# Optimization experiments

Measured on AMD Instinct MI355X. Metric: run time of the kernel, lower is better.

Reference implementation:

```python
import jax, jax.numpy as jnp
import numpy as np

NEG_SLOPE = 0.2  # init arg negative_slope


def setup_inputs() -> dict:
    key = jax.random.key(0)
    k1, k2, k3, k4 = jax.random.split(key, 4)
    N, E, D_IN, D_OUT = 8192, 262144, 128, 128
    h = jax.random.normal(k1, (N, D_IN), dtype=jnp.float32)
    edge_index = jax.random.randint(k2, (2, E), 0, N, dtype=jnp.int64)
    # nn.Linear(in, out, bias=False) weight: [out, in]
    W = jax.random.normal(k3, (D_OUT, D_IN), dtype=jnp.float32) * (1.0 / np.sqrt(D_IN))
    # att parameter: [2*out, 1], xavier-uniform-ish scale
    lim = np.sqrt(6.0 / (2 * D_OUT + 1)) * 1.414
    att = jax.random.uniform(k4, (2 * D_OUT, 1), dtype=jnp.float32, minval=-lim, maxval=lim)
    return {"h": h, "edge_index": edge_index, "W": W, "att": att}


def reference(h, edge_index, W, att):
    # h: [N, d_in], edge_index: [2, E], W: [d_out, d_in], att: [2*d_out, 1]
    h_trans = h @ W.T                                  # [N, d_out]
    row, col = edge_index[0], edge_index[1]
    e = jnp.concatenate([h_trans[row], h_trans[col]], axis=1)  # [E, 2*d_out]
    edge_e = jnp.squeeze(e @ att, axis=-1)             # [E]
    edge_e = jnp.where(edge_e >= 0, edge_e, NEG_SLOPE * edge_e)  # leaky_relu
    N = h.shape[0]
    attention = jnp.zeros((N, N), dtype=h_trans.dtype).at[row, col].set(edge_e)
    attention = (attention + attention.T) * 0.5        # symmetrize
    fill_value = edge_e.max()                          # .item() -> constant (no grad)
    diag = jnp.arange(N)
    attention = attention.at[diag, diag].set(fill_value)
    attention = jax.nn.softmax(attention, axis=1)      # row softmax over dense NxN
    h_prime = attention @ h_trans                      # [N, d_out]
    h_prime = jax.nn.elu(h_prime)                      # concat=True -> ELU
    # F.dropout in eval mode is identity
    return h_prime, attention
```

## Files before the change

kernel.cpp:

```cpp
#include <hip/hip_runtime.h>
#include <stdint.h>

#define NN 8192
#define EE 262144
#define DD 128
#define NEGS 0.2f
#define HBITS 20
#define HSIZE (1<<HBITS)
#define HMASK (HSIZE-1)
#define BCAP 256

typedef float f32x4 __attribute__((ext_vector_type(4)));

__device__ __forceinline__ unsigned f2ord(float f){
  unsigned u = __float_as_uint(f);
  return (u & 0x80000000u) ? ~u : (u | 0x80000000u);
}
__device__ __forceinline__ float ord2f(unsigned u){
  return __uint_as_float((u & 0x80000000u) ? (u & 0x7fffffffu) : ~u);
}
__device__ __forceinline__ unsigned hmix(int key){
  unsigned h = (unsigned)key * 2654435761u;
  h ^= h >> 15;
  return h;
}

__global__ void k_setup(int* hkeys, int* hvals, int* cnt, float* T,
                        unsigned* fillmax, const float* __restrict__ W,
                        float* __restrict__ wt){
  int gid = blockIdx.x*256 + threadIdx.x;
  int4 m1 = {-1,-1,-1,-1};
  if(gid < HSIZE/4)            ((int4*)hkeys)[gid] = m1;
  else if(gid < HSIZE/2)       ((int4*)hvals)[gid - HSIZE/4] = m1;
  if(gid < NN/4)               ((int4*)cnt)[gid] = int4{0,0,0,0};
  if(gid < DD/4)               ((float4*)T)[gid] = float4{0.f,0.f,0.f,0.f};
  if(gid == 0)                 *fillmax = 0x007FFFFFu;
  if(gid < DD*DD){
    int c = gid >> 7, k = gid & 127;
    wt[k*DD + c] = W[gid];
  }
}

__global__ __launch_bounds__(256) void k_gemm(const float* __restrict__ h,
                                              const float* __restrict__ wt,
                                              float* __restrict__ ht){
  __shared__ float wl[64*DD];
  __shared__ float hl[16][132];
  int t = threadIdx.x;
  int row0 = blockIdx.x * 16;
  #pragma unroll
  for(int u=0;u<2;u++){
    int f4 = u*256 + t;
    int r = f4 >> 5, k4 = f4 & 31;
    float4 v = ((const float4*)(h + (size_t)(row0+r)*DD))[k4];
    *((float4*)&hl[r][k4*4]) = v;
  }
  int r  = t & 15;
  int c0 = (t >> 4) * 8;
  float acc[8];
  #pragma unroll
  for(int s=0;s<8;s++) acc[s]=0.f;
  for(int p=0;p<2;p++){
    __syncthreads();
    const float4* wsrc = (const float4*)(wt + p*64*DD);
    float4* wd = (float4*)wl;
    #pragma unroll
    for(int u=0;u<8;u++) wd[u*256+t] = wsrc[u*256+t];
    __syncthreads();
    #pragma unroll 2
    for(int kk=0;kk<64;kk++){
      float hv = hl[r][p*64+kk];
      const float4* wr4 = (const float4*)&wl[kk*DD + c0];
      float4 w0 = wr4[0], w1 = wr4[1];
      acc[0] += hv*w0.x; acc[1] += hv*w0.y; acc[2] += hv*w0.z; acc[3] += hv*w0.w;
      acc[4] += hv*w1.x; acc[5] += hv*w1.y; acc[6] += hv*w1.z; acc[7] += hv*w1.w;
    }
  }
  float4* o = (float4*)(ht + (size_t)(row0+r)*DD + c0);
  o[0] = float4{acc[0],acc[1],acc[2],acc[3]};
  o[1] = float4{acc[4],acc[5],acc[6],acc[7]};
}

__global__ __launch_bounds__(256) void k_stats(const float* __restrict__ ht,
    const float* __restrict__ att, float* T, float* a1, float* a2){
  int t = threadIdx.x, b = blockIdx.x;
  int lane = t & 63;
  int i = b*4 + (t >> 6);
  const float* hr = ht + (size_t)i*DD;
  float h0 = hr[lane], h1 = hr[lane+64];
  float x1 = h0*att[lane]    + h1*att[lane+64];
  float x2 = h0*att[DD+lane] + h1*att[DD+lane+64];
  #pragma unroll
  for(int o=32;o>0;o>>=1){ x1 += __shfl_down(x1,o); x2 += __shfl_down(x2,o); }
  if(lane==0){ a1[i]=x1; a2[i]=x2; }
  if(b < 64){
    __shared__ float part[256];
    int c = t & 127, half = t >> 7;
    float s = 0.f;
    int r0 = b*128 + half*64;
    for(int rr=r0; rr<r0+64; rr++) s += ht[(size_t)rr*DD + c];
    part[t] = s; __syncthreads();
    if(half==0) atomicAdd(&T[c], part[t] + part[t+128]);
  }
}

__global__ void k_edge(const int* __restrict__ ei, const float* __restrict__ a1,
                       const float* __restrict__ a2, float* __restrict__ val,
                       unsigned* fillmax, int* hkeys, int* hvals){
  int k = blockIdx.x*256 + threadIdx.x;
  int r = ei[k], c = ei[EE + k];
  float e = a1[r] + a2[c];
  e = e >= 0.f ? e : NEGS*e;
  val[k] = e;
  float wm = e;
  #pragma unroll
  for(int o=32;o>0;o>>=1) wm = fmaxf(wm, __shfl_down(wm,o));
  __shared__ float sm[4];
  if((threadIdx.x & 63)==0) sm[threadIdx.x>>6] = wm;
  __syncthreads();
  if(threadIdx.x==0){
    float bm = fmaxf(fmaxf(sm[0],sm[1]), fmaxf(sm[2],sm[3]));
    atomicMax(fillmax, f2ord(bm));
  }
  if(r != c){
    int key = (r<<13) | c;
    unsigned slot = hmix(key) & HMASK;
    while(true){
      int prev = atomicCAS(&hkeys[slot], -1, key);
      if(prev == -1 || prev == key){ atomicMax(&hvals[slot], k); break; }
      slot = (slot + 1) & HMASK;
    }
  }
}

__global__ void k_fill(const int* __restrict__ hkeys, const int* __restrict__ hvals,
                       const float* __restrict__ val, int* cnt,
                       int2* __restrict__ bucket){
  int base = (blockIdx.x*256 + threadIdx.x) * 2;
  #pragma unroll
  for(int u=0;u<2;u++){
    int s = base + u;
    int key = hkeys[s];
    if(key < 0) continue;
    int i = key >> 13, j = key & (NN-1);
    int kwin = hvals[s];
    int rkey = (j<<13) | i;
    unsigned slot = hmix(rkey) & HMASK;
    int krev = -1;
    while(true){
      int kk = hkeys[slot];
      if(kk == rkey){ krev = hvals[slot]; break; }
      if(kk == -1) break;
      slot = (slot + 1) & HMASK;
    }
    float a = 0.5f * (val[kwin] + (krev >= 0 ? val[krev] : 0.f));
    int p = atomicAdd(&cnt[i], 1);
    if(p < BCAP) bucket[((size_t)i<<8) + p] = int2{j, __float_as_int(a)};
    if(krev < 0){
      int q = atomicAdd(&cnt[j], 1);
      if(q < BCAP) bucket[((size_t)j<<8) + q] = int2{i, __float_as_int(a)};
    }
  }
}

__global__ __launch_bounds__(256) void k_rowstats(const float* __restrict__ ht,
    const float* __restrict__ T, const int* __restrict__ cnt,
    const int2* __restrict__ bucket, const unsigned* __restrict__ fillmax,
    float* inv_, float* z_, float* dg_, float* __restrict__ hprime){
  int lane = threadIdx.x & 63;
  int i = blockIdx.x*4 + (threadIdx.x >> 6);
  float fill = ord2f(*fillmax);
  float m = fmaxf(fill, 0.f);
  int n = min(cnt[i], BCAP);
  const int2* brow = bucket + ((size_t)i<<8);
  float ds = 0.f;
  for(int e=lane; e<n; e+=64) ds += __expf(__int_as_float(brow[e].y) - m);
  #pragma unroll
  for(int o=32;o>0;o>>=1) ds += __shfl_xor(ds,o);
  float ez = __expf(-m);
  float ef = __expf(fill - m);
  float denom = ds + ef + (float)(NN-1-n)*ez;
  float invd = 1.f/denom;
  if(lane==0){ inv_[i]=invd; z_[i]=ez*invd; dg_[i]=ef*invd; }
  const float* hti = ht + (size_t)i*DD;
  float acc0 = ez*T[lane]    + (ef-ez)*hti[lane];
  float acc1 = ez*T[lane+64] + (ef-ez)*hti[lane+64];
  for(int e=0;e<n;e++){
    int2 be = brow[e];
    float w = __expf(__int_as_float(be.y) - m) - ez;
    const float* htj = ht + (size_t)be.x*DD;
    acc0 += w*htj[lane];
    acc1 += w*htj[lane+64];
  }
  acc0 *= invd; acc1 *= invd;
  acc0 = acc0 > 0.f ? acc0 : expm1f(acc0);
  acc1 = acc1 > 0.f ? acc1 : expm1f(acc1);
  hprime[(size_t)i*DD + lane]      = acc0;
  hprime[(size_t)i*DD + lane + 64] = acc1;
}

__global__ __launch_bounds__(256) void k_zfill(const float* __restrict__ z_,
                                               float* __restrict__ attn){
  int idx = blockIdx.x*256 + threadIdx.x;
  f32x4* o = (f32x4*)attn;
  #pragma unroll
  for(int u=0;u<16;u++){
    int f4i = idx + u*(4096*256);
    float z = z_[f4i >> 11];
    f32x4 v = {z,z,z,z};
    __builtin_nontemporal_store(v, o + f4i);
  }
}

__global__ void k_patch(const int* __restrict__ cnt, const int2* __restrict__ bucket,
                        const unsigned* __restrict__ fillmax,
                        const float* __restrict__ inv_, const float* __restrict__ dg_,
                        float* __restrict__ attn){
  int s = blockIdx.x*256 + threadIdx.x;
  int i = s >> 8, e = s & 255;
  float fill = ord2f(*fillmax);
  float m = fmaxf(fill, 0.f);
  int n = min(cnt[i], BCAP);
  if(e < n){
    int2 be = bucket[s];
    attn[((size_t)i<<13) + be.x] = __expf(__int_as_float(be.y) - m) * inv_[i];
  }
  if(s < NN) attn[((size_t)s<<13) + s] = dg_[s];
}

extern "C" void kernel_launch(void* const* d_in, const int* in_sizes, int n_in,
                              void* d_out, int out_size, void* d_ws, size_t ws_size,
                              hipStream_t stream){
  const float* h   = (const float*)d_in[0];
  const int*   ei  = (const int*)d_in[1];
  const float* W   = (const float*)d_in[2];
  const float* att = (const float*)d_in[3];
  float* out = (float*)d_out;
  float* hprime = out;
  float* attn   = out + (size_t)NN*DD;

  int*   hkeys = (int*)attn;
  int*   hvals = hkeys + HSIZE;
  float* val   = (float*)(hvals + HSIZE);
  float* a1    = val + EE;
  float* a2    = a1 + NN;

  char* ws = (char*)d_ws;
  size_t off = 0;
  auto alloc = [&](size_t bytes)->char*{
    char* p = ws + off;
    off = (off + bytes + 255) & ~(size_t)255;
    return p;
  };
  float* ht      = (float*)alloc((size_t)NN*DD*4);
  float* wt      = (float*)alloc((size_t)DD*DD*4);
  float* T       = (float*)alloc((size_t)DD*4);
  int*   cnt     = (int*)alloc((size_t)NN*4);
  float* inv_    = (float*)alloc((size_t)NN*4);
  float* z_      = (float*)alloc((size_t)NN*4);
  float* dg_     = (float*)alloc((size_t)NN*4);
  unsigned* fillmax = (unsigned*)alloc(256);
  int2*  bucket  = (int2*)alloc((size_t)NN*BCAP*8);

  k_setup   <<<2048, 256, 0, stream>>>(hkeys, hvals, cnt, T, fillmax, W, wt);
  k_gemm    <<<NN/16, 256, 0, stream>>>(h, wt, ht);
  k_stats   <<<NN/4, 256, 0, stream>>>(ht, att, T, a1, a2);
  k_edge    <<<EE/256, 256, 0, stream>>>(ei, a1, a2, val, fillmax, hkeys, hvals);
  k_fill    <<<HSIZE/512, 256, 0, stream>>>(hkeys, hvals, val, cnt, bucket);
  k_rowstats<<<NN/4, 256, 0, stream>>>(ht, T, cnt, bucket, fillmax, inv_, z_, dg_, hprime);
  k_zfill   <<<4096, 256, 0, stream>>>(z_, attn);
  k_patch   <<<NN*BCAP/256, 256, 0, stream>>>(cnt, bucket, fillmax, inv_, dg_, attn);
}
```

Baseline: 231.9 us.

## Fuse dense fill and sparse patch into one per-row shared-memory kernel

Replaces the separate zero-fill and scatter-patch kernels with one kernel that builds each attention row in LDS (fill with z, scatter edge values and the diagonal), then streams the row to global memory with nontemporal stores. This removes the second pass of scattered global writes over the 256 MB output and one kernel launch. The hash table is also halved (HBITS 20 to 19), with the setup grid reduced to match, which shrinks the setup and fill work but raises the load factor and probe lengths. Each block needs 32 KB of LDS, which may limit occupancy.

```diff
diff --git a/kernel.cpp b/kernel.cpp
--- a/kernel.cpp
+++ b/kernel.cpp
@@ -5,7 +5,7 @@
 #define EE 262144
 #define DD 128
 #define NEGS 0.2f
-#define HBITS 20
+#define HBITS 19
 #define HSIZE (1<<HBITS)
 #define HMASK (HSIZE-1)
 #define BCAP 256
@@ -199,33 +199,29 @@
   hprime[(size_t)i*DD + lane + 64] = acc1;
 }
 
-__global__ __launch_bounds__(256) void k_zfill(const float* __restrict__ z_,
-                                               float* __restrict__ attn){
-  int idx = blockIdx.x*256 + threadIdx.x;
-  f32x4* o = (f32x4*)attn;
-  #pragma unroll
-  for(int u=0;u<16;u++){
-    int f4i = idx + u*(4096*256);
-    float z = z_[f4i >> 11];
-    f32x4 v = {z,z,z,z};
-    __builtin_nontemporal_store(v, o + f4i);
-  }
-}
-
-__global__ void k_patch(const int* __restrict__ cnt, const int2* __restrict__ bucket,
-                        const unsigned* __restrict__ fillmax,
-                        const float* __restrict__ inv_, const float* __restrict__ dg_,
-                        float* __restrict__ attn){
-  int s = blockIdx.x*256 + threadIdx.x;
-  int i = s >> 8, e = s & 255;
-  float fill = ord2f(*fillmax);
-  float m = fmaxf(fill, 0.f);
+__global__ __launch_bounds__(256) void k_dense(const int* __restrict__ cnt,
+    const int2* __restrict__ bucket, const unsigned* __restrict__ fillmax,
+    const float* __restrict__ inv_, const float* __restrict__ z_,
+    const float* __restrict__ dg_, float* __restrict__ attn){
+  __shared__ float rowbuf[NN];
+  int i = blockIdx.x, t = threadIdx.x;
+  float z = z_[i];
+  f32x4 zv = {z,z,z,z};
+  f32x4* rb4 = (f32x4*)rowbuf;
+  #pragma unroll
+  for(int u=0;u<8;u++) rb4[u*256+t] = zv;
+  __syncthreads();
   int n = min(cnt[i], BCAP);
-  if(e < n){
-    int2 be = bucket[s];
-    attn[((size_t)i<<13) + be.x] = __expf(__int_as_float(be.y) - m) * inv_[i];
-  }
-  if(s < NN) attn[((size_t)s<<13) + s] = dg_[s];
+  if(t < n){
+    float m = fmaxf(ord2f(*fillmax), 0.f);
+    int2 be = bucket[((size_t)i<<8) + t];
+    rowbuf[be.x] = __expf(__int_as_float(be.y) - m) * inv_[i];
+  }
+  if(t==0) rowbuf[i] = dg_[i];
+  __syncthreads();
+  f32x4* o = (f32x4*)(attn + ((size_t)i<<13));
+  #pragma unroll
+  for(int u=0;u<8;u++) __builtin_nontemporal_store(rb4[u*256+t], o + u*256+t);
 }
 
 extern "C" void kernel_launch(void* const* d_in, const int* in_sizes, int n_in,
@@ -262,12 +258,11 @@
   unsigned* fillmax = (unsigned*)alloc(256);
   int2*  bucket  = (int2*)alloc((size_t)NN*BCAP*8);
 
-  k_setup   <<<2048, 256, 0, stream>>>(hkeys, hvals, cnt, T, fillmax, W, wt);
+  k_setup   <<<1024, 256, 0, stream>>>(hkeys, hvals, cnt, T, fillmax, W, wt);
   k_gemm    <<<NN/16, 256, 0, stream>>>(h, wt, ht);
   k_stats   <<<NN/4, 256, 0, stream>>>(ht, att, T, a1, a2);
   k_edge    <<<EE/256, 256, 0, stream>>>(ei, a1, a2, val, fillmax, hkeys, hvals);
   k_fill    <<<HSIZE/512, 256, 0, stream>>>(hkeys, hvals, val, cnt, bucket);
   k_rowstats<<<NN/4, 256, 0, stream>>>(ht, T, cnt, bucket, fillmax, inv_, z_, dg_, hprime);
-  k_zfill   <<<4096, 256, 0, stream>>>(z_, attn);
-  k_patch   <<<NN*BCAP/256, 256, 0, stream>>>(cnt, bucket, fillmax, inv_, dg_, attn);
-}
+  k_dense   <<<NN, 256, 0, stream>>>(cnt, bucket, fillmax, inv_, z_, dg_, attn);
+}
```

After: 204.9 us, median of 2. 11.6% less time.
